# Optimization experiments

Measured on AMD Instinct MI355X. Metric: run time of the kernel, lower is better.

## Reference

```python
import jax, jax.numpy as jnp
import numpy as np

DIM = 768
NUM_HEADS = 12
HEAD_DIM = DIM // NUM_HEADS
WS = 14                       # window_size (14, 14)
N_TOK = WS * WS + 1           # 197 (patches + cls)
NUM_REL = (2 * WS - 1) ** 2 + 3  # 732
SCALE = HEAD_DIM ** -0.5


def _build_rel_index():
    # Faithful port of the BEiT relative_position_index construction.
    coords = np.stack(np.meshgrid(np.arange(WS), np.arange(WS), indexing='ij'))  # (2, WS, WS)
    flat = coords.reshape(2, -1)                                   # (2, WS*WS)
    rel = flat[:, :, None] - flat[:, None, :]                      # (2, P, P)
    rel = rel.transpose(1, 2, 0).astype(np.int64)                  # (P, P, 2)
    rel[:, :, 0] += WS - 1
    rel[:, :, 1] += WS - 1
    rel[:, :, 0] *= 2 * WS - 1
    idx = np.zeros((N_TOK, N_TOK), dtype=np.int64)
    idx[1:, 1:] = rel.sum(-1)
    idx[0, :] = NUM_REL - 3
    idx[:, 0] = NUM_REL - 2
    idx[0, 0] = NUM_REL - 1
    return idx


def setup_inputs() -> dict:
    key = jax.random.key(0)
    ks = jax.random.split(key, 7)
    B = 64
    x = jax.random.normal(ks[0], (B, N_TOK, DIM), dtype=jnp.float32)
    qkv_w = jax.random.normal(ks[1], (3 * DIM, DIM), dtype=jnp.float32) * 0.02
    q_bias = jnp.zeros((DIM,), dtype=jnp.float32)
    v_bias = jnp.zeros((DIM,), dtype=jnp.float32)
    rel_table = jax.random.normal(ks[2], (NUM_REL, NUM_HEADS), dtype=jnp.float32) * 0.02
    proj_w = jax.random.normal(ks[3], (DIM, DIM), dtype=jnp.float32) * 0.02
    proj_b = jnp.zeros((DIM,), dtype=jnp.float32)
    rel_index = jnp.asarray(_build_rel_index())  # (N, N) int64
    return {"x": x, "qkv_w": qkv_w, "q_bias": q_bias, "v_bias": v_bias,
            "rel_table": rel_table, "proj_w": proj_w, "proj_b": proj_b,
            "rel_index": rel_index}


def reference(x, qkv_w, q_bias, v_bias, rel_table, proj_w, proj_b, rel_index):
    B, N, C = x.shape
    # qkv bias = concat(q_bias, zeros, v_bias)
    qkv_b = jnp.concatenate([q_bias, jnp.zeros_like(v_bias), v_bias])
    qkv = x @ qkv_w.T + qkv_b                       # (B, N, 3C)
    qkv = qkv.reshape(B, N, 3, NUM_HEADS, HEAD_DIM).transpose(2, 0, 3, 1, 4)
    q, k, v = qkv[0], qkv[1], qkv[2]                # each (B, H, N, hd)
    attn = jnp.einsum('bhqd,bhkd->bhqk', q * SCALE, k)
    # relative position bias gathered from table: (N, N, H) -> (H, N, N)
    bias = rel_table[rel_index].transpose(2, 0, 1)
    attn = attn + bias[None]
    attn = jax.nn.softmax(attn, axis=-1)
    out = jnp.einsum('bhqk,bhkd->bhqd', attn, v)    # (B, H, N, hd)
    out = out.transpose(0, 2, 1, 3).reshape(B, N, -1)
    return out @ proj_w.T + proj_b
```

## Files before the change

kernel.cpp:

```cpp
#include <hip/hip_runtime.h>
#include <stdint.h>

#define NTOK 197
#define HD 64
#define NH 12
#define CDIM 768
#define BB 64
#define MTOT (BB*NTOK)
#define MPAD 12672
#define SCALE 0.125f

typedef __attribute__((ext_vector_type(8))) short short8;
typedef __attribute__((ext_vector_type(4))) float f32x4;
typedef unsigned short us;

__device__ __forceinline__ us f2b(float f){
    union { float f; uint32_t u; } v; v.f = f;
    uint32_t u = v.u;
    uint32_t r = u + 0x7fffu + ((u >> 16) & 1u);
    return (us)(r >> 16);
}

__device__ __forceinline__ float b2f(us b){
    union { uint32_t u; float f; } v; v.u = ((uint32_t)b) << 16;
    return v.f;
}

__device__ __forceinline__ void gload16(const us* g, us* l){
    __builtin_amdgcn_global_load_lds((const __attribute__((address_space(1))) void*)g,
                                     (__attribute__((address_space(3))) void*)l, 16, 0, 0);
}

__global__ void cvt_kernel(const float* __restrict__ in, us* __restrict__ out, int n4){
    int i = blockIdx.x*blockDim.x + threadIdx.x;
    if (i < n4){
        float4 v = ((const float4*)in)[i];
        ushort4 o;
        o.x = f2b(v.x); o.y = f2b(v.y); o.z = f2b(v.z); o.w = f2b(v.w);
        ((ushort4*)out)[i] = o;
    }
}

__global__ void bias_kernel(const int* __restrict__ rel_index, const float* __restrict__ rel_table,
                            float* __restrict__ biasm){
    int i = blockIdx.x*blockDim.x + threadIdx.x;
    if (i < NTOK*NTOK){
        int idx = rel_index[i];
        #pragma unroll
        for (int h = 0; h < NH; ++h)
            biasm[h*NTOK*NTOK + i] = rel_table[idx*NH + h];
    }
}

template<int EPI, int TPB>
__global__ __launch_bounds__(256) void pgemm_kernel(
    const us* __restrict__ A, const us* __restrict__ Bw,
    float* __restrict__ Cout, us* __restrict__ Qo, us* __restrict__ Ko, us* __restrict__ Vo,
    const float* __restrict__ b0, const float* __restrict__ b2, int ny)
{
    __shared__ __align__(16) us lds[32768];
    us* As = lds;
    us* Bs = lds + 16384;
    const int tid  = threadIdx.x;
    const int lane = tid & 63;
    const int wave = tid >> 6;
    const int wr = wave >> 1, wc = wave & 1;
    const int lr = lane & 15;
    const int g  = lane >> 4;

    const int NB   = gridDim.x;
    const int base = NB >> 3;
    const int rem  = NB & 7;
    const int id   = blockIdx.x;
    const int xcd  = id & 7;
    const int qq   = id >> 3;
    const int start = (xcd < rem) ? xcd*(base+1) : rem*(base+1) + (xcd-rem)*base;
    const int w0   = (start + qq) * TPB;

    const int row0 = tid >> 4;
    const int cg   = (tid & 15) ^ row0;
    const int NT   = CDIM / 128;

    #pragma unroll 1
    for (int tt = 0; tt < TPB; ++tt){
        const int w  = w0 + tt;
        const int bx = w / ny;
        const int by = w - bx*ny;
        const int m0 = bx * 128;
        const int n0 = by * 128;
        const int which = (EPI == 0) ? (n0 >> 9) / ((768*2) >> 10) : 0;
        const int whc = (EPI == 0) ? (n0 / CDIM) : 0;

        float addf[4], sclf[4];
        #pragma unroll
        for (int nt=0;nt<4;nt++){
            int n = n0 + wc*64 + nt*16 + lr;
            if (EPI == 1){ addf[nt] = b0[n]; sclf[nt] = 1.f; }
            else {
                int hn = n - whc*CDIM;
                if (whc == 0){ addf[nt] = b0[hn]; sclf[nt] = SCALE; }
                else if (whc == 1){ addf[nt] = 0.f; sclf[nt] = 1.f; }
                else { addf[nt] = b2[hn]; sclf[nt] = 1.f; }
            }
        }

        f32x4 acc[4][4];
        #pragma unroll
        for (int i=0;i<4;i++)
            #pragma unroll
            for (int j=0;j<4;j++) acc[i][j] = (f32x4){0.f,0.f,0.f,0.f};

        const us* gA = A  + (size_t)(m0 + row0)*CDIM + cg*8;
        const us* gB = Bw + (size_t)(n0 + row0)*CDIM + cg*8;

        #pragma unroll 1
        for (int kt = 0; kt < NT; ++kt){
            __syncthreads();
            #pragma unroll
            for (int j=0;j<8;j++){
                gload16(gA + (size_t)j*16*CDIM + kt*128, As + tid*8 + j*2048);
                gload16(gB + (size_t)j*16*CDIM + kt*128, Bs + tid*8 + j*2048);
            }
            __syncthreads();
            #pragma unroll
            for (int kk=0; kk<4; ++kk){
                const int co = 8*((kk*4 + g) ^ lr);
                short8 af[4], bf[4];
                #pragma unroll
                for (int mt=0;mt<4;mt++)
                    af[mt] = *(const short8*)&As[(wr*64+mt*16+lr)*128 + co];
                #pragma unroll
                for (int nt=0;nt<4;nt++)
                    bf[nt] = *(const short8*)&Bs[(wc*64+nt*16+lr)*128 + co];
                __builtin_amdgcn_s_setprio(1);
                #pragma unroll
                for (int mt=0;mt<4;mt++)
                    #pragma unroll
                    for (int nt=0;nt<4;nt++)
                        acc[mt][nt] = __builtin_amdgcn_mfma_f32_16x16x32_bf16(af[mt], bf[nt], acc[mt][nt], 0,0,0);
                __builtin_amdgcn_s_setprio(0);
            }
        }

        __syncthreads();
        #pragma unroll
        for (int mt=0;mt<4;mt++)
            #pragma unroll
            for (int r=0;r<4;r++){
                int row = wr*64 + mt*16 + g*4 + r;
                #pragma unroll
                for (int nt=0;nt<4;nt++){
                    int col = wc*64 + nt*16 + lr;
                    lds[row*132 + col] = f2b((acc[mt][nt][r] + addf[nt]) * sclf[nt]);
                }
            }
        __syncthreads();
        const us* outp = (EPI == 0) ? (whc == 0 ? Qo : (whc == 1 ? Ko : Vo)) : nullptr;
        #pragma unroll
        for (int j=0;j<8;j++){
            int c2  = tid + j*256;
            int row = c2 >> 4;
            int ch  = c2 & 15;
            int m = m0 + row;
            if (m >= MTOT) continue;
            short8 vv = *(const short8*)&lds[row*132 + ch*8];
            if (EPI == 1){
                int n = n0 + ch*8;
                float4 f0, f1;
                f0.x = b2f((us)vv[0]); f0.y = b2f((us)vv[1]); f0.z = b2f((us)vv[2]); f0.w = b2f((us)vv[3]);
                f1.x = b2f((us)vv[4]); f1.y = b2f((us)vv[5]); f1.z = b2f((us)vv[6]); f1.w = b2f((us)vv[7]);
                *(float4*)&Cout[(size_t)m*CDIM + n]     = f0;
                *(float4*)&Cout[(size_t)m*CDIM + n + 4] = f1;
            } else {
                int n  = n0 + ch*8;
                int hn = n - whc*CDIM;
                int h  = hn >> 6, d0 = hn & 63;
                int bidx = m / NTOK;
                int tok  = m - bidx*NTOK;
                size_t off = ((size_t)((bidx*NH + h)*NTOK + tok))*HD + d0;
                *(short8*)((us*)outp + off) = vv;
            }
        }
    }
}

__global__ __launch_bounds__(256) void attn_kernel(
    const us* __restrict__ Q,
    const us* __restrict__ K,
    const us* __restrict__ V,
    const float* __restrict__ biasm,
    us* __restrict__ Ao)
{
    __shared__ us Vt[64][232];
    __shared__ us Ps[4][16][232];
    const int bh = blockIdx.x;
    const int b = bh / NH;
    const int h = bh - b*NH;
    const us* Qh = Q + (size_t)bh*NTOK*HD;
    const us* Kh = K + (size_t)bh*NTOK*HD;
    const us* Vh = V + (size_t)bh*NTOK*HD;
    const float* bh_bias = biasm + (size_t)h*NTOK*NTOK;
    const int tid = threadIdx.x, lane = tid & 63, wave = tid >> 6;
    const int lr = lane & 15, g = lane >> 4, ko = g*8;

    for (int i = tid; i < 64*232/2; i += 256) ((uint32_t*)Vt)[i] = 0;
    __syncthreads();
    {
        int d0 = (tid & 7) * 8;
        for (int t = tid >> 3; t < NTOK; t += 32){
            short8 v = *(const short8*)&Vh[t*HD + d0];
            #pragma unroll
            for (int j=0;j<8;j++) Vt[d0+j][t] = (us)v[j];
        }
    }
    __syncthreads();

    for (int s = wave; s < 13; s += 4){
        int qrow = s*16 + lr; qrow = qrow > 196 ? 196 : qrow;
        short8 qa0 = *(const short8*)&Qh[qrow*HD + ko];
        short8 qa1 = *(const short8*)&Qh[qrow*HD + 32 + ko];
        f32x4 S[13];
        #pragma unroll
        for (int t=0;t<13;t++){
            int kc = t*16 + lr; kc = kc > 196 ? 196 : kc;
            short8 kb0 = *(const short8*)&Kh[kc*HD + ko];
            short8 kb1 = *(const short8*)&Kh[kc*HD + 32 + ko];
            f32x4 a = (f32x4){0.f,0.f,0.f,0.f};
            a = __builtin_amdgcn_mfma_f32_16x16x32_bf16(qa0, kb0, a, 0,0,0);
            a = __builtin_amdgcn_mfma_f32_16x16x32_bf16(qa1, kb1, a, 0,0,0);
            S[t] = a;
        }
        float rmax[4] = {-3e38f,-3e38f,-3e38f,-3e38f};
        #pragma unroll
        for (int t=0;t<13;t++){
            int col = t*16 + lr;
            bool cok = col < NTOK;
            int colc = cok ? col : 196;
            #pragma unroll
            for (int r=0;r<4;r++){
                int row = s*16 + g*4 + r; row = row > 196 ? 196 : row;
                float xv = S[t][r] + bh_bias[row*NTOK + colc];
                xv = cok ? xv : -1e30f;
                S[t][r] = xv;
                rmax[r] = fmaxf(rmax[r], xv);
            }
        }
        #pragma unroll
        for (int r=0;r<4;r++)
            #pragma unroll
            for (int msk=1; msk<16; msk<<=1)
                rmax[r] = fmaxf(rmax[r], __shfl_xor(rmax[r], msk));
        float rsum[4] = {0.f,0.f,0.f,0.f};
        #pragma unroll
        for (int t=0;t<13;t++)
            #pragma unroll
            for (int r=0;r<4;r++){
                float e = __expf(S[t][r] - rmax[r]);
                S[t][r] = e;
                rsum[r] += e;
            }
        #pragma unroll
        for (int r=0;r<4;r++){
            #pragma unroll
            for (int msk=1; msk<16; msk<<=1)
                rsum[r] += __shfl_xor(rsum[r], msk);
            rsum[r] = 1.f / rsum[r];
        }
        #pragma unroll
        for (int t=0;t<13;t++)
            #pragma unroll
            for (int r=0;r<4;r++)
                Ps[wave][g*4+r][t*16+lr] = f2b(S[t][r] * rsum[r]);
        #pragma unroll
        for (int r=0;r<4;r++) Ps[wave][g*4+r][208+lr] = 0;
        asm volatile("s_waitcnt lgkmcnt(0)" ::: "memory");
        f32x4 pv[4];
        #pragma unroll
        for (int nt=0;nt<4;nt++) pv[nt] = (f32x4){0.f,0.f,0.f,0.f};
        #pragma unroll
        for (int ks=0; ks<7; ks++){
            int k0 = ks*32 + ko;
            short8 pa = *(const short8*)&Ps[wave][lr][k0];
            #pragma unroll
            for (int nt=0;nt<4;nt++){
                short8 vb = *(const short8*)&Vt[nt*16+lr][k0];
                pv[nt] = __builtin_amdgcn_mfma_f32_16x16x32_bf16(pa, vb, pv[nt], 0,0,0);
            }
        }
        #pragma unroll
        for (int nt=0;nt<4;nt++)
            #pragma unroll
            for (int r=0;r<4;r++){
                int tok = s*16 + g*4 + r;
                if (tok < NTOK)
                    Ao[(size_t)(b*NTOK + tok)*CDIM + h*HD + nt*16 + lr] = f2b(pv[nt][r]);
            }
    }
}

extern "C" void kernel_launch(void* const* d_in, const int* in_sizes, int n_in,
                              void* d_out, int out_size, void* d_ws, size_t ws_size,
                              hipStream_t stream)
{
    const float* x        = (const float*)d_in[0];
    const float* qkv_w    = (const float*)d_in[1];
    const float* q_bias   = (const float*)d_in[2];
    const float* v_bias   = (const float*)d_in[3];
    const float* rel_tab  = (const float*)d_in[4];
    const float* proj_w   = (const float*)d_in[5];
    const float* proj_b   = (const float*)d_in[6];
    const int*   rel_idx  = (const int*)d_in[7];
    float* out = (float*)d_out;

    char* w = (char*)d_ws;
    us* xb    = (us*)w; w += (size_t)MPAD*CDIM*2;
    us* wqkv  = (us*)w; w += (size_t)3*CDIM*CDIM*2;
    us* wproj = (us*)w; w += (size_t)CDIM*CDIM*2;
    us* Qb    = (us*)w; w += (size_t)BB*NH*NTOK*HD*2;
    us* Kb    = (us*)w; w += (size_t)BB*NH*NTOK*HD*2;
    us* Vb    = (us*)w; w += (size_t)BB*NH*NTOK*HD*2;
    float* biasm = (float*)w; w += (size_t)NH*NTOK*NTOK*4;
    us* aob   = (us*)w; w += (size_t)MPAD*CDIM*2;

    int n1 = MTOT*CDIM/4;
    cvt_kernel<<<(n1+255)/256, 256, 0, stream>>>(x, xb, n1);
    int n2 = 3*CDIM*CDIM/4;
    cvt_kernel<<<(n2+255)/256, 256, 0, stream>>>(qkv_w, wqkv, n2);
    int n3 = CDIM*CDIM/4;
    cvt_kernel<<<(n3+255)/256, 256, 0, stream>>>(proj_w, wproj, n3);
    bias_kernel<<<(NTOK*NTOK+255)/256, 256, 0, stream>>>(rel_idx, rel_tab, biasm);

    pgemm_kernel<0,3><<<594, 256, 0, stream>>>(xb, wqkv, nullptr, Qb, Kb, Vb, q_bias, v_bias, 18);
    attn_kernel<<<BB*NH, 256, 0, stream>>>(Qb, Kb, Vb, biasm, aob);
    pgemm_kernel<1,1><<<594, 256, 0, stream>>>(aob, wproj, out, nullptr, nullptr, nullptr, proj_b, nullptr, 6);
}
```

Baseline: 176.5 us.

## Rewrite GEMMs as persistent double-buffered 128x256 tile kernel with 512 threads

Replaces the QKV and projection GEMM kernel with a persistent kernel of 256 blocks that split the tile list evenly. Each block computes 128x256 tiles with 8 waves and double-buffers LDS stages of 64 K-elements, prefetching the next K slice or the next tile's first slice while computing. This removes the load-then-compute serialization and the XCD-remapped grid of the old kernel. It costs a larger LDS footprint and one block per CU, and the epilogue is now written in two halves with extra barriers.

Measured after the change: 199.1 us. 1.13x slower.

```diff
diff --git a/kernel.cpp b/kernel.cpp
--- a/kernel.cpp
+++ b/kernel.cpp
@@ -52,55 +52,77 @@
     }
 }
 
-template<int EPI, int TPB>
-__global__ __launch_bounds__(256) void pgemm_kernel(
+template<int EPI>
+__global__ __launch_bounds__(512,1) void pgemm2_kernel(
     const us* __restrict__ A, const us* __restrict__ Bw,
     float* __restrict__ Cout, us* __restrict__ Qo, us* __restrict__ Ko, us* __restrict__ Vo,
-    const float* __restrict__ b0, const float* __restrict__ b2, int ny)
+    const float* __restrict__ b0, const float* __restrict__ b2, int ny, int total)
 {
-    __shared__ __align__(16) us lds[32768];
-    us* As = lds;
-    us* Bs = lds + 16384;
+    __shared__ __align__(16) us AsB[2][24576];
+    __shared__ __align__(16) us cbuf[128*132];
     const int tid  = threadIdx.x;
     const int lane = tid & 63;
     const int wave = tid >> 6;
-    const int wr = wave >> 1, wc = wave & 1;
+    const int wrr = wave >> 2;
+    const int wcc = wave & 3;
     const int lr = lane & 15;
     const int g  = lane >> 4;
 
-    const int NB   = gridDim.x;
-    const int base = NB >> 3;
-    const int rem  = NB & 7;
-    const int id   = blockIdx.x;
-    const int xcd  = id & 7;
-    const int qq   = id >> 3;
-    const int start = (xcd < rem) ? xcd*(base+1) : rem*(base+1) + (xcd-rem)*base;
-    const int w0   = (start + qq) * TPB;
-
-    const int row0 = tid >> 4;
-    const int cg   = (tid & 15) ^ row0;
-    const int NT   = CDIM / 128;
+    const int id = blockIdx.x, NB = gridDim.x;
+    const int q  = total / NB, r = total - q*NB;
+    const int cnt = q + (id < r ? 1 : 0);
+    const int w0  = id*q + (id < r ? id : r);
+    if (cnt == 0) return;
+
+    int aoff[2], bofs[4];
+    int aldo[2], bldo[4];
+    #pragma unroll
+    for (int p=0;p<2;p++){
+        int c = tid + p*512;
+        int row = c >> 3, ch = c & 7;
+        aoff[p] = row*CDIM + ((ch ^ (row & 7))*8);
+        aldo[p] = c*8;
+    }
+    #pragma unroll
+    for (int j=0;j<4;j++){
+        int c = tid + j*512;
+        int row = c >> 3, ch = c & 7;
+        bofs[j] = row*CDIM + ((ch ^ (row & 7))*8);
+        bldo[j] = 8192 + c*8;
+    }
+
+    auto stage = [&](int buf, const us* pA, const us* pB, int kt){
+        #pragma unroll
+        for (int p=0;p<2;p++) gload16(pA + aoff[p] + kt*64, &AsB[buf][aldo[p]]);
+        #pragma unroll
+        for (int j=0;j<4;j++) gload16(pB + bofs[j] + kt*64, &AsB[buf][bldo[j]]);
+    };
+
+    int w  = w0;
+    int bx = w / ny, by = w - bx*ny;
+    int m0 = bx*128, n0 = by*256;
+    const us* pA = A  + (size_t)m0*CDIM;
+    const us* pB = Bw + (size_t)n0*CDIM;
+    stage(0, pA, pB, 0);
+    int buf = 0;
 
     #pragma unroll 1
-    for (int tt = 0; tt < TPB; ++tt){
-        const int w  = w0 + tt;
-        const int bx = w / ny;
-        const int by = w - bx*ny;
-        const int m0 = bx * 128;
-        const int n0 = by * 128;
-        const int which = (EPI == 0) ? (n0 >> 9) / ((768*2) >> 10) : 0;
+    for (int tt = 0; tt < cnt; ++tt){
+        int w1 = w + 1;
+        int bx1 = w1 / ny, by1 = w1 - bx1*ny;
+        const us* pA1 = A  + (size_t)(bx1*128)*CDIM;
+        const us* pB1 = Bw + (size_t)(by1*256)*CDIM;
+
         const int whc = (EPI == 0) ? (n0 / CDIM) : 0;
-
-        float addf[4], sclf[4];
+        float addf[4], sclf;
+        sclf = (EPI == 0 && whc == 0) ? SCALE : 1.f;
         #pragma unroll
         for (int nt=0;nt<4;nt++){
-            int n = n0 + wc*64 + nt*16 + lr;
-            if (EPI == 1){ addf[nt] = b0[n]; sclf[nt] = 1.f; }
+            int n = n0 + wcc*64 + nt*16 + lr;
+            if (EPI == 1) addf[nt] = b0[n];
             else {
                 int hn = n - whc*CDIM;
-                if (whc == 0){ addf[nt] = b0[hn]; sclf[nt] = SCALE; }
-                else if (whc == 1){ addf[nt] = 0.f; sclf[nt] = 1.f; }
-                else { addf[nt] = b2[hn]; sclf[nt] = 1.f; }
+                addf[nt] = (whc == 0) ? b0[hn] : (whc == 2 ? b2[hn] : 0.f);
             }
         }
 
@@ -110,28 +132,24 @@
             #pragma unroll
             for (int j=0;j<4;j++) acc[i][j] = (f32x4){0.f,0.f,0.f,0.f};
 
-        const us* gA = A  + (size_t)(m0 + row0)*CDIM + cg*8;
-        const us* gB = Bw + (size_t)(n0 + row0)*CDIM + cg*8;
-
         #pragma unroll 1
-        for (int kt = 0; kt < NT; ++kt){
-            __syncthreads();
-            #pragma unroll
-            for (int j=0;j<8;j++){
-                gload16(gA + (size_t)j*16*CDIM + kt*128, As + tid*8 + j*2048);
-                gload16(gB + (size_t)j*16*CDIM + kt*128, Bs + tid*8 + j*2048);
-            }
-            __syncthreads();
-            #pragma unroll
-            for (int kk=0; kk<4; ++kk){
-                const int co = 8*((kk*4 + g) ^ lr);
+        for (int kt = 0; kt < 12; ++kt){
+            asm volatile("s_waitcnt vmcnt(0)" ::: "memory");
+            __builtin_amdgcn_s_barrier();
+            if (kt < 11)           stage(buf^1, pA,  pB,  kt+1);
+            else if (tt+1 < cnt)   stage(buf^1, pA1, pB1, 0);
+            const us* la = &AsB[buf][0];
+            const us* lb = &AsB[buf][8192];
+            #pragma unroll
+            for (int kk=0; kk<2; ++kk){
+                const int co = 8*((kk*4 + g) ^ (lr & 7));
                 short8 af[4], bf[4];
                 #pragma unroll
                 for (int mt=0;mt<4;mt++)
-                    af[mt] = *(const short8*)&As[(wr*64+mt*16+lr)*128 + co];
+                    af[mt] = *(const short8*)&la[(wrr*64+mt*16+lr)*64 + co];
                 #pragma unroll
                 for (int nt=0;nt<4;nt++)
-                    bf[nt] = *(const short8*)&Bs[(wc*64+nt*16+lr)*128 + co];
+                    bf[nt] = *(const short8*)&lb[(wcc*64+nt*16+lr)*64 + co];
                 __builtin_amdgcn_s_setprio(1);
                 #pragma unroll
                 for (int mt=0;mt<4;mt++)
@@ -140,47 +158,54 @@
                         acc[mt][nt] = __builtin_amdgcn_mfma_f32_16x16x32_bf16(af[mt], bf[nt], acc[mt][nt], 0,0,0);
                 __builtin_amdgcn_s_setprio(0);
             }
-        }
-
-        __syncthreads();
-        #pragma unroll
-        for (int mt=0;mt<4;mt++)
-            #pragma unroll
-            for (int r=0;r<4;r++){
-                int row = wr*64 + mt*16 + g*4 + r;
+            buf ^= 1;
+        }
+
+        const us* outp = (EPI == 0) ? (whc == 0 ? Qo : (whc == 1 ? Ko : Vo)) : nullptr;
+        #pragma unroll 1
+        for (int half = 0; half < 2; ++half){
+            if ((wcc >> 1) == half){
                 #pragma unroll
-                for (int nt=0;nt<4;nt++){
-                    int col = wc*64 + nt*16 + lr;
-                    lds[row*132 + col] = f2b((acc[mt][nt][r] + addf[nt]) * sclf[nt]);
+                for (int mt=0;mt<4;mt++)
+                    #pragma unroll
+                    for (int rr=0;rr<4;rr++){
+                        int row = wrr*64 + mt*16 + g*4 + rr;
+                        #pragma unroll
+                        for (int nt=0;nt<4;nt++){
+                            int col = (wcc & 1)*64 + nt*16 + lr;
+                            cbuf[row*132 + col] = f2b((acc[mt][nt][rr] + addf[nt]) * sclf);
+                        }
+                    }
+            }
+            __syncthreads();
+            #pragma unroll
+            for (int p=0;p<4;p++){
+                int c = tid + p*512;
+                int row = c >> 4, ch = c & 15;
+                int m = m0 + row;
+                if (m < MTOT){
+                    short8 vv = *(const short8*)&cbuf[row*132 + ch*8];
+                    int n = n0 + half*128 + ch*8;
+                    if (EPI == 1){
+                        float4 f0, f1;
+                        f0.x = b2f((us)vv[0]); f0.y = b2f((us)vv[1]); f0.z = b2f((us)vv[2]); f0.w = b2f((us)vv[3]);
+                        f1.x = b2f((us)vv[4]); f1.y = b2f((us)vv[5]); f1.z = b2f((us)vv[6]); f1.w = b2f((us)vv[7]);
+                        *(float4*)&Cout[(size_t)m*CDIM + n]     = f0;
+                        *(float4*)&Cout[(size_t)m*CDIM + n + 4] = f1;
+                    } else {
+                        int hn = n - whc*CDIM;
+                        int h  = hn >> 6, d0 = hn & 63;
+                        int bidx = m / NTOK;
+                        int tok  = m - bidx*NTOK;
+                        size_t off = ((size_t)((bidx*NH + h)*NTOK + tok))*HD + d0;
+                        *(short8*)((us*)outp + off) = vv;
+                    }
                 }
             }
-        __syncthreads();
-        const us* outp = (EPI == 0) ? (whc == 0 ? Qo : (whc == 1 ? Ko : Vo)) : nullptr;
-        #pragma unroll
-        for (int j=0;j<8;j++){
-            int c2  = tid + j*256;
-            int row = c2 >> 4;
-            int ch  = c2 & 15;
-            int m = m0 + row;
-            if (m >= MTOT) continue;
-            short8 vv = *(const short8*)&lds[row*132 + ch*8];
-            if (EPI == 1){
-                int n = n0 + ch*8;
-                float4 f0, f1;
-                f0.x = b2f((us)vv[0]); f0.y = b2f((us)vv[1]); f0.z = b2f((us)vv[2]); f0.w = b2f((us)vv[3]);
-                f1.x = b2f((us)vv[4]); f1.y = b2f((us)vv[5]); f1.z = b2f((us)vv[6]); f1.w = b2f((us)vv[7]);
-                *(float4*)&Cout[(size_t)m*CDIM + n]     = f0;
-                *(float4*)&Cout[(size_t)m*CDIM + n + 4] = f1;
-            } else {
-                int n  = n0 + ch*8;
-                int hn = n - whc*CDIM;
-                int h  = hn >> 6, d0 = hn & 63;
-                int bidx = m / NTOK;
-                int tok  = m - bidx*NTOK;
-                size_t off = ((size_t)((bidx*NH + h)*NTOK + tok))*HD + d0;
-                *(short8*)((us*)outp + off) = vv;
-            }
-        }
+            __syncthreads();
+        }
+
+        w = w1; bx = bx1; by = by1; m0 = bx1*128; n0 = by1*256; pA = pA1; pB = pB1;
     }
 }
 
@@ -330,7 +355,7 @@
     cvt_kernel<<<(n3+255)/256, 256, 0, stream>>>(proj_w, wproj, n3);
     bias_kernel<<<(NTOK*NTOK+255)/256, 256, 0, stream>>>(rel_idx, rel_tab, biasm);
 
-    pgemm_kernel<0,3><<<594, 256, 0, stream>>>(xb, wqkv, nullptr, Qb, Kb, Vb, q_bias, v_bias, 18);
+    pgemm2_kernel<0><<<256, 512, 0, stream>>>(xb, wqkv, nullptr, Qb, Kb, Vb, q_bias, v_bias, 9, 891);
     attn_kernel<<<BB*NH, 256, 0, stream>>>(Qb, Kb, Vb, biasm, aob);
-    pgemm_kernel<1,1><<<594, 256, 0, stream>>>(aob, wproj, out, nullptr, nullptr, nullptr, proj_b, nullptr, 6);
-}
+    pgemm2_kernel<1><<<256, 512, 0, stream>>>(aob, wproj, out, nullptr, nullptr, nullptr, proj_b, nullptr, 3, 297);
+}
```
